# Performance work log

Hardware: AMD Instinct MI355X
Metric: run time of the kernel (lower is better)

Reference implementation:

```python
import jax, jax.numpy as jnp
import numpy as np

B, T, E, H = 4, 2048, 1024, 16
HS = E // H  # 64
EPS = 1e-5


def _layernorm(x, g, b):
    mu = jnp.mean(x, axis=-1, keepdims=True)
    var = jnp.mean(jnp.square(x - mu), axis=-1, keepdims=True)
    return (x - mu) * jax.lax.rsqrt(var + EPS) * g + b


def setup_inputs() -> dict:
    key = jax.random.key(0)
    ks = jax.random.split(key, 12)
    s = 0.02
    return {
        "x": jax.random.normal(ks[0], (B, T, E), dtype=jnp.float32),
        "ln1_g": jnp.ones((E,), jnp.float32),
        "ln1_b": jnp.zeros((E,), jnp.float32),
        "Wq": jax.random.normal(ks[1], (H, E, HS), jnp.float32) * s,
        "Wk": jax.random.normal(ks[2], (H, E, HS), jnp.float32) * s,
        "Wv": jax.random.normal(ks[3], (H, E, HS), jnp.float32) * s,
        "Wo": jax.random.normal(ks[4], (E, E), jnp.float32) * s,
        "bo": jnp.zeros((E,), jnp.float32),
        "ln2_g": jnp.ones((E,), jnp.float32),
        "ln2_b": jnp.zeros((E,), jnp.float32),
        "W1": jax.random.normal(ks[5], (E, 4 * E), jnp.float32) * s,
        "b1": jnp.zeros((4 * E,), jnp.float32),
        "W2": jax.random.normal(ks[6], (4 * E, E), jnp.float32) * s,
        "b2": jnp.zeros((E,), jnp.float32),
    }


def reference(x, ln1_g, ln1_b, Wq, Wk, Wv, Wo, bo, ln2_g, ln2_b, W1, b1, W2, b2):
    # --- self-attention (pre-LN) ---
    h = _layernorm(x, ln1_g, ln1_b)                      # [B,T,E]
    q = jnp.einsum('bte,hed->bhtd', h, Wq)               # [B,H,T,HS]
    k = jnp.einsum('bte,hed->bhtd', h, Wk)
    v = jnp.einsum('bte,hed->bhtd', h, Wv)
    scores = jnp.einsum('bhtd,bhsd->bhts', q, k) * (HS ** -0.5)  # [B,H,T,T]
    att = jax.nn.softmax(scores, axis=-1)
    o = jnp.einsum('bhts,bhsd->bhtd', att, v)            # [B,H,T,HS]
    o = jnp.transpose(o, (0, 2, 1, 3)).reshape(B, T, E)  # concat heads
    x = x + o @ Wo + bo                                  # residual
    # --- feed-forward (pre-LN) ---
    h2 = _layernorm(x, ln2_g, ln2_b)
    x = x + jax.nn.relu(h2 @ W1 + b1) @ W2 + b2
    return x
```

## Files before the change

kernel.cpp:

```cpp
#include <hip/hip_runtime.h>
#include <stdint.h>


typedef __attribute__((ext_vector_type(8))) short s16x8;
typedef __attribute__((ext_vector_type(4))) float f32x4;
typedef unsigned short u16;
typedef __attribute__((ext_vector_type(4))) unsigned short u16x4;

#define XSW(r) ((((r) & 7) ^ (((r) >> 3) & 7)) << 4)

__device__ __forceinline__ u16 f2bf(float f) {
    uint32_t u = __float_as_uint(f);
    u += 0x7fffu + ((u >> 16) & 1u);
    return (u16)(u >> 16);
}
__device__ __forceinline__ float bf2f(u16 u) {
    return __uint_as_float(((uint32_t)u) << 16);
}
__device__ __forceinline__ uint32_t pk2(float a, float b) {
    return (uint32_t)f2bf(a) | ((uint32_t)f2bf(b) << 16);
}
__device__ __forceinline__ float exp2_fast(float x) {
    float r;
    asm("v_exp_f32 %0, %1" : "=v"(r) : "v"(x));
    return r;
}

__device__ __forceinline__ void gld16(const void* g, void* l) {
    __builtin_amdgcn_global_load_lds(
        (const __attribute__((address_space(1))) unsigned int*)g,
        (__attribute__((address_space(3))) unsigned int*)l, 16, 0, 0);
}

__global__ __launch_bounds__(256)
void ln_bf16(const float* __restrict__ x, const float* __restrict__ g,
             const float* __restrict__ bta, u16* __restrict__ y) {
    __shared__ float red[8];
    const int row = blockIdx.x;
    const int t = threadIdx.x;
    const float4 xv = ((const float4*)(x + (size_t)row * 1024))[t];
    float s = xv.x + xv.y + xv.z + xv.w;
    float q = xv.x*xv.x + xv.y*xv.y + xv.z*xv.z + xv.w*xv.w;
#pragma unroll
    for (int off = 32; off; off >>= 1) {
        s += __shfl_down(s, off, 64);
        q += __shfl_down(q, off, 64);
    }
    if ((t & 63) == 0) { red[(t>>6)*2] = s; red[(t>>6)*2+1] = q; }
    __syncthreads();
    const float st = red[0]+red[2]+red[4]+red[6];
    const float qt = red[1]+red[3]+red[5]+red[7];
    const float mu = st * (1.f/1024.f);
    const float rs = rsqrtf(qt*(1.f/1024.f) - mu*mu + 1e-5f);
    const float4 gv = ((const float4*)g)[t];
    const float4 bv = ((const float4*)bta)[t];
    u16x4 o;
    o.x = f2bf((xv.x-mu)*rs*gv.x + bv.x);
    o.y = f2bf((xv.y-mu)*rs*gv.y + bv.y);
    o.z = f2bf((xv.z-mu)*rs*gv.z + bv.z);
    o.w = f2bf((xv.w-mu)*rs*gv.w + bv.w);
    ((u16x4*)(y + (size_t)row*1024))[t] = o;
}

__global__ __launch_bounds__(256)
void transpose_f32_bf16(const float* __restrict__ in, u16* __restrict__ out,
                        int K, int N) {
    __shared__ float tile[64][65];
    const int k0 = blockIdx.x * 64;
    const int n0 = blockIdx.y * 64;
    const int t = threadIdx.x;
    const int r = t >> 2;
    const int c = (t & 3) * 16;
    const float* ip = in + (size_t)(k0 + r) * N + n0 + c;
#pragma unroll
    for (int i = 0; i < 4; ++i) {
        const float4 v = *(const float4*)(ip + i*4);
        tile[r][c+i*4+0]=v.x; tile[r][c+i*4+1]=v.y;
        tile[r][c+i*4+2]=v.z; tile[r][c+i*4+3]=v.w;
    }
    __syncthreads();
    u16 tmp[16] __attribute__((aligned(16)));
#pragma unroll
    for (int i = 0; i < 16; ++i) tmp[i] = f2bf(tile[c+i][r]);
    u16* op = out + (size_t)(n0 + r) * K + k0 + c;
    *(s16x8*)op       = *(const s16x8*)&tmp[0];
    *(s16x8*)(op + 8) = *(const s16x8*)&tmp[8];
}

__global__ __launch_bounds__(256)
void pack_wcat(const float* __restrict__ Wq, const float* __restrict__ Wk,
               const float* __restrict__ Wv, u16* __restrict__ out) {
    __shared__ float tile[64][65];
    const int ph = blockIdx.y;
    const int p = ph >> 4, h = ph & 15;
    const float* W = (p == 0) ? Wq : (p == 1 ? Wk : Wv);
    const float* in = W + (size_t)h * 64 * 1024;
    const int k0 = blockIdx.x * 64;
    const int t = threadIdx.x;
    const int r = t >> 2;
    const int c = (t & 3) * 16;
    const float* ip = in + (size_t)(k0 + r) * 64 + c;
#pragma unroll
    for (int i = 0; i < 4; ++i) {
        const float4 v = *(const float4*)(ip + i*4);
        tile[r][c+i*4+0]=v.x; tile[r][c+i*4+1]=v.y;
        tile[r][c+i*4+2]=v.z; tile[r][c+i*4+3]=v.w;
    }
    __syncthreads();
    u16 tmp[16] __attribute__((aligned(16)));
#pragma unroll
    for (int i = 0; i < 16; ++i) tmp[i] = f2bf(tile[c+i][r]);
    u16* op = out + (size_t)(p*1024 + h*64 + r) * 1024 + k0 + c;
    *(s16x8*)op       = *(const s16x8*)&tmp[0];
    *(s16x8*)(op + 8) = *(const s16x8*)&tmp[8];
}

template<bool RELU, bool HAS_BIAS, bool HAS_RES, bool OUT_BF16, bool SPLIT_V>
__global__ __launch_bounds__(256)
void bgemm(const u16* __restrict__ A, int lda,
           const u16* __restrict__ Bt, int ldb,
           void* Cv, int ldc,
           const float* __restrict__ bias,
           const float* Res, int ldres, int K,
           u16* __restrict__ vT)
{
    __shared__ u16 Als[128*64];
    __shared__ u16 Bls[128*64];
    const int tid = threadIdx.x;
    const int wid = tid >> 6, lane = tid & 63;
    const int bm = blockIdx.y * 128, bn = blockIdx.x * 128;
    const int wr = (wid >> 1) * 64, wc = (wid & 1) * 64;
    const int fr = lane & 15, fq = lane >> 4;
    const int sr8 = lane >> 3, sc8 = (lane & 7) * 8;

    const f32x4 zero = {0.f, 0.f, 0.f, 0.f};
    f32x4 acc[4][4];
#pragma unroll
    for (int m = 0; m < 4; ++m)
#pragma unroll
        for (int n = 0; n < 4; ++n) acc[m][n] = zero;

    const u16* Ap = A  + (size_t)(bm + wid*32 + sr8) * lda + sc8;
    const u16* Bp = Bt + (size_t)(bn + wid*32 + sr8) * ldb + sc8;
    u16* Alp = Als + wid*2048 + lane*8;
    u16* Blp = Bls + wid*2048 + lane*8;

    for (int k0 = 0; k0 < K; k0 += 64) {
#pragma unroll
        for (int c = 0; c < 4; ++c) {
            gld16(Ap + (size_t)(c*8)*lda + k0, Alp + c*512);
            gld16(Bp + (size_t)(c*8)*ldb + k0, Blp + c*512);
        }
        __syncthreads();
#pragma unroll
        for (int kk = 0; kk < 2; ++kk) {
            s16x8 af[4], bf[4];
#pragma unroll
            for (int m = 0; m < 4; ++m)
                af[m] = *(const s16x8*)((const char*)Als + (wr+m*16+fr)*128 + kk*64 + fq*16);
#pragma unroll
            for (int n = 0; n < 4; ++n)
                bf[n] = *(const s16x8*)((const char*)Bls + (wc+n*16+fr)*128 + kk*64 + fq*16);
#pragma unroll
            for (int m = 0; m < 4; ++m)
#pragma unroll
                for (int n = 0; n < 4; ++n)
                    acc[m][n] = __builtin_amdgcn_mfma_f32_16x16x32_bf16(
                        af[m], bf[n], acc[m][n], 0, 0, 0);
        }
        __syncthreads();
    }

    float* Cf = (float*)Cv;
    u16*  Cb = (u16*)Cv;
    if (SPLIT_V && bn >= 2048) {
#pragma unroll
        for (int n = 0; n < 4; ++n) {
            const int local = bn + wc + n*16 + fr - 2048;
            const int hh = local >> 6, dd = local & 63;
#pragma unroll
            for (int m = 0; m < 4; ++m) {
#pragma unroll
                for (int j = 0; j < 4; ++j) {
                    const int row = bm + wr + m*16 + fq*4 + j;
                    const int bb = row >> 11, tt = row & 2047;
                    vT[((size_t)(bb*16 + hh)*64 + dd)*2048 + tt] = f2bf(acc[m][n][j]);
                }
            }
        }
        return;
    }
#pragma unroll
    for (int n = 0; n < 4; ++n) {
        const int col = bn + wc + n*16 + fr;
        const float bval = HAS_BIAS ? bias[col] : 0.f;
#pragma unroll
        for (int m = 0; m < 4; ++m) {
#pragma unroll
            for (int j = 0; j < 4; ++j) {
                const int row = bm + wr + m*16 + fq*4 + j;
                float v = acc[m][n][j] + bval;
                if (HAS_RES) v += Res[(size_t)row * ldres + col];
                if (RELU)    v = fmaxf(v, 0.f);
                if (OUT_BF16) Cb[(size_t)row * ldc + col] = f2bf(v);
                else          Cf[(size_t)row * ldc + col] = v;
            }
        }
    }
}

__global__ __launch_bounds__(256)
void attn_bf16(const u16* __restrict__ qk, const u16* __restrict__ vT,
               u16* __restrict__ out) {
    __shared__ u16 Ks[128*64];
    __shared__ u16 Vt[64*128];
    __shared__ u16 Ps[4][16*128];
    const int b = blockIdx.y >> 4, h = blockIdx.y & 15;
    const int q0 = blockIdx.x << 6;
    const int tid = threadIdx.x;
    const int wid = tid >> 6, lane = tid & 63;
    const int fr = lane & 15, fq = lane >> 4;
    const int srow = tid >> 2;
    const int sce  = (tid & 3) * 16;
    const int vd   = tid >> 4;
    const int vt0  = (tid & 15) * 8;
    const size_t tokbase = (size_t)b * 2048;
    const u16* vbase = vT + (size_t)(b*16 + h) * 64 * 2048;
    const f32x4 zero = {0.f, 0.f, 0.f, 0.f};

    u16* Qst = (u16*)Ps;
    {
        const u16* qp = qk + (tokbase + q0 + srow)*2048 + h*64 + sce;
        const s16x8 v0 = *(const s16x8*)qp;
        const s16x8 v1 = *(const s16x8*)(qp + 8);
        *(s16x8*)((char*)Qst + srow*128 + ((sce*2)      ^ XSW(srow))) = v0;
        *(s16x8*)((char*)Qst + srow*128 + ((sce*2 + 16) ^ XSW(srow))) = v1;
    }
    __syncthreads();
    s16x8 qf[2];
    {
        const int qrow = wid*16 + fr;
        const float qscale = 0.125f * 1.44269504f;
#pragma unroll
        for (int kk = 0; kk < 2; ++kk) {
            const s16x8 raw = *(const s16x8*)((const char*)Qst + qrow*128
                                 + ((kk*64 + fq*16) ^ XSW(qrow)));
#pragma unroll
            for (int i = 0; i < 8; ++i)
                qf[kk][i] = (short)f2bf(bf2f((u16)raw[i]) * qscale);
        }
    }

    float m_run = -1e30f, l_run = 0.f;
    f32x4 oacc[4];
#pragma unroll
    for (int nd = 0; nd < 4; ++nd) oacc[nd] = zero;

    s16x8 kr[4], vr[4];
    {
        const u16* kp0 = qk + (tokbase + srow)*2048 + 1024 + h*64 + sce;
        kr[0] = *(const s16x8*)kp0;
        kr[1] = *(const s16x8*)(kp0 + 8);
        kr[2] = *(const s16x8*)(kp0 + (size_t)64*2048);
        kr[3] = *(const s16x8*)(kp0 + (size_t)64*2048 + 8);
#pragma unroll
        for (int c = 0; c < 4; ++c)
            vr[c] = *(const s16x8*)(vbase + (size_t)(vd + 16*c)*2048 + vt0);
    }

    for (int kt = 0; kt < 2048; kt += 128) {
        __syncthreads();
        {
            const int r0 = srow, r1 = srow + 64;
            *(s16x8*)((char*)Ks + r0*128 + ((sce*2)      ^ XSW(r0))) = kr[0];
            *(s16x8*)((char*)Ks + r0*128 + ((sce*2 + 16) ^ XSW(r0))) = kr[1];
            *(s16x8*)((char*)Ks + r1*128 + ((sce*2)      ^ XSW(r1))) = kr[2];
            *(s16x8*)((char*)Ks + r1*128 + ((sce*2 + 16) ^ XSW(r1))) = kr[3];
        }
#pragma unroll
        for (int c = 0; c < 4; ++c) {
            const int d = vd + 16*c;
            *(s16x8*)((char*)Vt + d*256 + ((vt0*2) ^ XSW(d))) = vr[c];
        }
        __syncthreads();

        if (kt + 128 < 2048) {
            const u16* kp0 = qk + (tokbase + kt + 128 + srow)*2048 + 1024 + h*64 + sce;
            kr[0] = *(const s16x8*)kp0;
            kr[1] = *(const s16x8*)(kp0 + 8);
            kr[2] = *(const s16x8*)(kp0 + (size_t)64*2048);
            kr[3] = *(const s16x8*)(kp0 + (size_t)64*2048 + 8);
#pragma unroll
            for (int c = 0; c < 4; ++c)
                vr[c] = *(const s16x8*)(vbase + (size_t)(vd + 16*c)*2048
                                        + kt + 128 + vt0);
        }

        f32x4 sv[8];
        __builtin_amdgcn_s_setprio(1);
#pragma unroll
        for (int n = 0; n < 8; ++n) {
            sv[n] = zero;
            const int r = n*16 + fr;
#pragma unroll
            for (int kk = 0; kk < 2; ++kk) {
                const s16x8 kf = *(const s16x8*)((const char*)Ks + r*128
                                     + ((kk*64 + fq*16) ^ XSW(r)));
                sv[n] = __builtin_amdgcn_mfma_f32_16x16x32_bf16(kf, qf[kk], sv[n], 0,0,0);
            }
        }
        __builtin_amdgcn_s_setprio(0);

        float pv[32];
        float mx = -1e30f;
#pragma unroll
        for (int n = 0; n < 8; ++n)
#pragma unroll
            for (int j = 0; j < 4; ++j) {
                const float s = sv[n][j];
                pv[n*4 + j] = s;
                mx = fmaxf(mx, s);
            }
        mx = fmaxf(mx, __shfl_xor(mx, 16, 64));
        mx = fmaxf(mx, __shfl_xor(mx, 32, 64));
        const float mn = fmaxf(m_run, mx);
        const float al = exp2_fast(m_run - mn);
        m_run = mn;
        float rs = 0.f;
#pragma unroll
        for (int t = 0; t < 32; ++t) { pv[t] = exp2_fast(pv[t] - mn); rs += pv[t]; }
        rs += __shfl_xor(rs, 16, 64);
        rs += __shfl_xor(rs, 32, 64);
        l_run = l_run * al + rs;
#pragma unroll
        for (int nd = 0; nd < 4; ++nd)
#pragma unroll
            for (int j = 0; j < 4; ++j) oacc[nd][j] *= al;

        u16* Pw = (u16*)Ps + wid*2048;
#pragma unroll
        for (int n = 0; n < 8; ++n) {
            const uint64_t w = (uint64_t)pk2(pv[n*4+0], pv[n*4+1])
                             | ((uint64_t)pk2(pv[n*4+2], pv[n*4+3]) << 32);
            *(uint64_t*)((char*)Pw + fr*256 + ((n*32 + fq*8) ^ XSW(fr))) = w;
        }
        asm volatile("s_waitcnt lgkmcnt(0)" ::: "memory");
        __builtin_amdgcn_sched_barrier(0);

        s16x8 pf[4];
#pragma unroll
        for (int k2 = 0; k2 < 4; ++k2)
            pf[k2] = *(const s16x8*)((const char*)Pw + fr*256
                         + ((k2*64 + fq*16) ^ XSW(fr)));
        __builtin_amdgcn_s_setprio(1);
#pragma unroll
        for (int nd = 0; nd < 4; ++nd) {
            const int d = nd*16 + fr;
#pragma unroll
            for (int k2 = 0; k2 < 4; ++k2) {
                const s16x8 vf = *(const s16x8*)((const char*)Vt + d*256
                                     + ((k2*64 + fq*16) ^ XSW(d)));
                oacc[nd] = __builtin_amdgcn_mfma_f32_16x16x32_bf16(vf, pf[k2], oacc[nd], 0,0,0);
            }
        }
        __builtin_amdgcn_s_setprio(0);
    }

    const float inv = 1.0f / l_run;
    const size_t row = tokbase + q0 + wid*16 + fr;
#pragma unroll
    for (int nd = 0; nd < 4; ++nd) {
        u16x4 o;
#pragma unroll
        for (int j = 0; j < 4; ++j) o[j] = f2bf(oacc[nd][j] * inv);
        *(u16x4*)(out + row*1024 + h*64 + nd*16 + fq*4) = o;
    }
}

extern "C" void kernel_launch(void* const* d_in, const int* in_sizes, int n_in,
                              void* d_out, int out_size, void* d_ws, size_t ws_size,
                              hipStream_t stream) {
    (void)in_sizes; (void)n_in; (void)out_size; (void)ws_size;
    const float* x     = (const float*)d_in[0];
    const float* ln1_g = (const float*)d_in[1];
    const float* ln1_b = (const float*)d_in[2];
    const float* Wq    = (const float*)d_in[3];
    const float* Wk    = (const float*)d_in[4];
    const float* Wv    = (const float*)d_in[5];
    const float* Wo    = (const float*)d_in[6];
    const float* bo    = (const float*)d_in[7];
    const float* ln2_g = (const float*)d_in[8];
    const float* ln2_b = (const float*)d_in[9];
    const float* W1    = (const float*)d_in[10];
    const float* b1    = (const float*)d_in[11];
    const float* W2    = (const float*)d_in[12];
    const float* b2    = (const float*)d_in[13];
    float* out = (float*)d_out;

    char* w = (char*)d_ws;
    u16* WcatT = (u16*)w;  w += (size_t)3072*1024*2;
    u16* WoT   = (u16*)w;  w += (size_t)1024*1024*2;
    u16* W1T   = (u16*)w;  w += (size_t)4096*1024*2;
    u16* W2T   = (u16*)w;  w += (size_t)1024*4096*2;
    u16* hb    = (u16*)w;  w += (size_t)8192*1024*2;
    u16* qkb   = (u16*)w;  w += (size_t)8192*2048*2;
    u16* vTb   = (u16*)w;  w += (size_t)64*64*2048*2;
    u16* attno = (u16*)w;  w += (size_t)8192*1024*2;
    u16* a1    = (u16*)w;  w += (size_t)8192*4096*2;

    pack_wcat<<<dim3(16, 48), 256, 0, stream>>>(Wq, Wk, Wv, WcatT);
    transpose_f32_bf16<<<dim3(16, 16), 256, 0, stream>>>(Wo, WoT, 1024, 1024);
    transpose_f32_bf16<<<dim3(16, 64), 256, 0, stream>>>(W1, W1T, 1024, 4096);
    transpose_f32_bf16<<<dim3(64, 16), 256, 0, stream>>>(W2, W2T, 4096, 1024);

    ln_bf16<<<dim3(8192), 256, 0, stream>>>(x, ln1_g, ln1_b, hb);
    bgemm<false,false,false,true,true><<<dim3(24, 64), 256, 0, stream>>>(
        hb, 1024, WcatT, 1024, qkb, 2048, nullptr, nullptr, 0, 1024, vTb);
    attn_bf16<<<dim3(32, 64), 256, 0, stream>>>(qkb, vTb, attno);
    bgemm<false,true,true,false,false><<<dim3(8, 64), 256, 0, stream>>>(
        attno, 1024, WoT, 1024, out, 1024, bo, x, 1024, 1024, nullptr);
    ln_bf16<<<dim3(8192), 256, 0, stream>>>(out, ln2_g, ln2_b, hb);
    bgemm<true,true,false,true,false><<<dim3(32, 64), 256, 0, stream>>>(
        hb, 1024, W1T, 1024, a1, 4096, b1, nullptr, 0, 1024, nullptr);
    bgemm<false,true,true,false,false><<<dim3(8, 64), 256, 0, stream>>>(
        a1, 4096, W2T, 4096, out, 1024, b2, out, 1024, 4096, nullptr);
}
```

Measured before the change: 640.5 us.

## Load attention K/V directly from global, remap blocks for L2 locality, use hw bf16 pack

The attention kernel no longer stages K and V tiles through LDS with barriers. Each wave reads its MFMA fragments straight from global memory and relies on L2 reuse, with blocks of the same head remapped so they run close together in time. The GEMM block index is also remapped for L2 locality. Online softmax now rescales only when the running max grows by more than a threshold, and bf16 packing uses the hardware cvt_pk instruction. The risks are uncoalesced global fragment loads in place of LDS reads, and possible L2 or XCD locality effects from the remapping.

```diff
diff --git a/kernel.cpp b/kernel.cpp
--- a/kernel.cpp
+++ b/kernel.cpp
@@ -17,8 +17,10 @@
 __device__ __forceinline__ float bf2f(u16 u) {
     return __uint_as_float(((uint32_t)u) << 16);
 }
-__device__ __forceinline__ uint32_t pk2(float a, float b) {
-    return (uint32_t)f2bf(a) | ((uint32_t)f2bf(b) << 16);
+__device__ __forceinline__ uint32_t cvtpk(float a, float b) {
+    uint32_t r;
+    asm("v_cvt_pk_bf16_f32 %0, %1, %2" : "=v"(r) : "v"(a), "v"(b));
+    return r;
 }
 __device__ __forceinline__ float exp2_fast(float x) {
     float r;
@@ -54,12 +56,10 @@
     const float rs = rsqrtf(qt*(1.f/1024.f) - mu*mu + 1e-5f);
     const float4 gv = ((const float4*)g)[t];
     const float4 bv = ((const float4*)bta)[t];
-    u16x4 o;
-    o.x = f2bf((xv.x-mu)*rs*gv.x + bv.x);
-    o.y = f2bf((xv.y-mu)*rs*gv.y + bv.y);
-    o.z = f2bf((xv.z-mu)*rs*gv.z + bv.z);
-    o.w = f2bf((xv.w-mu)*rs*gv.w + bv.w);
-    ((u16x4*)(y + (size_t)row*1024))[t] = o;
+    uint32_t w0 = cvtpk((xv.x-mu)*rs*gv.x + bv.x, (xv.y-mu)*rs*gv.y + bv.y);
+    uint32_t w1 = cvtpk((xv.z-mu)*rs*gv.z + bv.z, (xv.w-mu)*rs*gv.w + bv.w);
+    uint2 o; o.x = w0; o.y = w1;
+    ((uint2*)(y + (size_t)row*1024))[t] = o;
 }
 
 __global__ __launch_bounds__(256)
@@ -128,7 +128,10 @@
     __shared__ u16 Bls[128*64];
     const int tid = threadIdx.x;
     const int wid = tid >> 6, lane = tid & 63;
-    const int bm = blockIdx.y * 128, bn = blockIdx.x * 128;
+    const int lin = blockIdx.y * gridDim.x + blockIdx.x;
+    const int qx = gridDim.x >> 3;
+    const int bn = ((lin & 7)*qx + ((lin >> 3) % qx)) * 128;
+    const int bm = ((lin >> 3) / qx) * 128;
     const int wr = (wid >> 1) * 64, wc = (wid & 1) * 64;
     const int fr = lane & 15, fq = lane >> 4;
     const int sr8 = lane >> 3, sc8 = (lane & 7) * 8;
@@ -212,42 +215,32 @@
 __global__ __launch_bounds__(256)
 void attn_bf16(const u16* __restrict__ qk, const u16* __restrict__ vT,
                u16* __restrict__ out) {
-    __shared__ u16 Ks[128*64];
-    __shared__ u16 Vt[64*128];
     __shared__ u16 Ps[4][16*128];
-    const int b = blockIdx.y >> 4, h = blockIdx.y & 15;
-    const int q0 = blockIdx.x << 6;
+    const int lin = blockIdx.x;
+    const int bh = (lin & 7)*8 + ((lin >> 3) & 7);
+    const int qb = lin >> 6;
+    const int b = bh >> 4, h = bh & 15;
+    const int q0 = qb << 6;
     const int tid = threadIdx.x;
     const int wid = tid >> 6, lane = tid & 63;
     const int fr = lane & 15, fq = lane >> 4;
-    const int srow = tid >> 2;
-    const int sce  = (tid & 3) * 16;
-    const int vd   = tid >> 4;
-    const int vt0  = (tid & 15) * 8;
     const size_t tokbase = (size_t)b * 2048;
     const u16* vbase = vT + (size_t)(b*16 + h) * 64 * 2048;
     const f32x4 zero = {0.f, 0.f, 0.f, 0.f};
-
-    u16* Qst = (u16*)Ps;
-    {
-        const u16* qp = qk + (tokbase + q0 + srow)*2048 + h*64 + sce;
-        const s16x8 v0 = *(const s16x8*)qp;
-        const s16x8 v1 = *(const s16x8*)(qp + 8);
-        *(s16x8*)((char*)Qst + srow*128 + ((sce*2)      ^ XSW(srow))) = v0;
-        *(s16x8*)((char*)Qst + srow*128 + ((sce*2 + 16) ^ XSW(srow))) = v1;
-    }
-    __syncthreads();
+    const float THR = 10.0f;
+
     s16x8 qf[2];
     {
-        const int qrow = wid*16 + fr;
-        const float qscale = 0.125f * 1.44269504f;
+        const u16* qp = qk + (tokbase + q0 + wid*16 + fr)*2048 + h*64;
+        const float qs = 0.125f * 1.44269504f;
 #pragma unroll
         for (int kk = 0; kk < 2; ++kk) {
-            const s16x8 raw = *(const s16x8*)((const char*)Qst + qrow*128
-                                 + ((kk*64 + fq*16) ^ XSW(qrow)));
-#pragma unroll
-            for (int i = 0; i < 8; ++i)
-                qf[kk][i] = (short)f2bf(bf2f((u16)raw[i]) * qscale);
+            const s16x8 raw = *(const s16x8*)(qp + kk*32 + fq*8);
+            union { s16x8 v; uint32_t w[4]; } u;
+#pragma unroll
+            for (int i = 0; i < 4; ++i)
+                u.w[i] = cvtpk(bf2f((u16)raw[2*i])*qs, bf2f((u16)raw[2*i+1])*qs);
+            qf[kk] = u.v;
         }
     }
 
@@ -256,56 +249,17 @@
 #pragma unroll
     for (int nd = 0; nd < 4; ++nd) oacc[nd] = zero;
 
-    s16x8 kr[4], vr[4];
-    {
-        const u16* kp0 = qk + (tokbase + srow)*2048 + 1024 + h*64 + sce;
-        kr[0] = *(const s16x8*)kp0;
-        kr[1] = *(const s16x8*)(kp0 + 8);
-        kr[2] = *(const s16x8*)(kp0 + (size_t)64*2048);
-        kr[3] = *(const s16x8*)(kp0 + (size_t)64*2048 + 8);
-#pragma unroll
-        for (int c = 0; c < 4; ++c)
-            vr[c] = *(const s16x8*)(vbase + (size_t)(vd + 16*c)*2048 + vt0);
-    }
-
     for (int kt = 0; kt < 2048; kt += 128) {
-        __syncthreads();
-        {
-            const int r0 = srow, r1 = srow + 64;
-            *(s16x8*)((char*)Ks + r0*128 + ((sce*2)      ^ XSW(r0))) = kr[0];
-            *(s16x8*)((char*)Ks + r0*128 + ((sce*2 + 16) ^ XSW(r0))) = kr[1];
-            *(s16x8*)((char*)Ks + r1*128 + ((sce*2)      ^ XSW(r1))) = kr[2];
-            *(s16x8*)((char*)Ks + r1*128 + ((sce*2 + 16) ^ XSW(r1))) = kr[3];
-        }
-#pragma unroll
-        for (int c = 0; c < 4; ++c) {
-            const int d = vd + 16*c;
-            *(s16x8*)((char*)Vt + d*256 + ((vt0*2) ^ XSW(d))) = vr[c];
-        }
-        __syncthreads();
-
-        if (kt + 128 < 2048) {
-            const u16* kp0 = qk + (tokbase + kt + 128 + srow)*2048 + 1024 + h*64 + sce;
-            kr[0] = *(const s16x8*)kp0;
-            kr[1] = *(const s16x8*)(kp0 + 8);
-            kr[2] = *(const s16x8*)(kp0 + (size_t)64*2048);
-            kr[3] = *(const s16x8*)(kp0 + (size_t)64*2048 + 8);
-#pragma unroll
-            for (int c = 0; c < 4; ++c)
-                vr[c] = *(const s16x8*)(vbase + (size_t)(vd + 16*c)*2048
-                                        + kt + 128 + vt0);
-        }
-
+        const u16* kp = qk + (tokbase + kt + fr)*2048 + 1024 + h*64 + fq*8;
         f32x4 sv[8];
         __builtin_amdgcn_s_setprio(1);
 #pragma unroll
         for (int n = 0; n < 8; ++n) {
             sv[n] = zero;
-            const int r = n*16 + fr;
+            const u16* kr = kp + (size_t)(n*16)*2048;
 #pragma unroll
             for (int kk = 0; kk < 2; ++kk) {
-                const s16x8 kf = *(const s16x8*)((const char*)Ks + r*128
-                                     + ((kk*64 + fq*16) ^ XSW(r)));
+                const s16x8 kf = *(const s16x8*)(kr + kk*32);
                 sv[n] = __builtin_amdgcn_mfma_f32_16x16x32_bf16(kf, qf[kk], sv[n], 0,0,0);
             }
         }
@@ -323,25 +277,27 @@
             }
         mx = fmaxf(mx, __shfl_xor(mx, 16, 64));
         mx = fmaxf(mx, __shfl_xor(mx, 32, 64));
-        const float mn = fmaxf(m_run, mx);
-        const float al = exp2_fast(m_run - mn);
-        m_run = mn;
+        if (mx > m_run + THR) {
+            const float al = exp2_fast(m_run - mx);
+            m_run = mx;
+            l_run *= al;
+#pragma unroll
+            for (int nd = 0; nd < 4; ++nd)
+#pragma unroll
+                for (int j = 0; j < 4; ++j) oacc[nd][j] *= al;
+        }
         float rs = 0.f;
 #pragma unroll
-        for (int t = 0; t < 32; ++t) { pv[t] = exp2_fast(pv[t] - mn); rs += pv[t]; }
+        for (int t = 0; t < 32; ++t) { pv[t] = exp2_fast(pv[t] - m_run); rs += pv[t]; }
         rs += __shfl_xor(rs, 16, 64);
         rs += __shfl_xor(rs, 32, 64);
-        l_run = l_run * al + rs;
-#pragma unroll
-        for (int nd = 0; nd < 4; ++nd)
-#pragma unroll
-            for (int j = 0; j < 4; ++j) oacc[nd][j] *= al;
+        l_run += rs;
 
         u16* Pw = (u16*)Ps + wid*2048;
 #pragma unroll
         for (int n = 0; n < 8; ++n) {
-            const uint64_t w = (uint64_t)pk2(pv[n*4+0], pv[n*4+1])
-                             | ((uint64_t)pk2(pv[n*4+2], pv[n*4+3]) << 32);
+            const uint64_t w = (uint64_t)cvtpk(pv[n*4+0], pv[n*4+1])
+                             | ((uint64_t)cvtpk(pv[n*4+2], pv[n*4+3]) << 32);
             *(uint64_t*)((char*)Pw + fr*256 + ((n*32 + fq*8) ^ XSW(fr))) = w;
         }
         asm volatile("s_waitcnt lgkmcnt(0)" ::: "memory");
@@ -352,14 +308,14 @@
         for (int k2 = 0; k2 < 4; ++k2)
             pf[k2] = *(const s16x8*)((const char*)Pw + fr*256
                          + ((k2*64 + fq*16) ^ XSW(fr)));
+        const u16* vp = vbase + (size_t)fr*2048 + kt + fq*8;
         __builtin_amdgcn_s_setprio(1);
 #pragma unroll
         for (int nd = 0; nd < 4; ++nd) {
-            const int d = nd*16 + fr;
+            const u16* vr = vp + (size_t)(nd*16)*2048;
 #pragma unroll
             for (int k2 = 0; k2 < 4; ++k2) {
-                const s16x8 vf = *(const s16x8*)((const char*)Vt + d*256
-                                     + ((k2*64 + fq*16) ^ XSW(d)));
+                const s16x8 vf = *(const s16x8*)(vr + k2*32);
                 oacc[nd] = __builtin_amdgcn_mfma_f32_16x16x32_bf16(vf, pf[k2], oacc[nd], 0,0,0);
             }
         }
@@ -370,10 +326,10 @@
     const size_t row = tokbase + q0 + wid*16 + fr;
 #pragma unroll
     for (int nd = 0; nd < 4; ++nd) {
-        u16x4 o;
-#pragma unroll
-        for (int j = 0; j < 4; ++j) o[j] = f2bf(oacc[nd][j] * inv);
-        *(u16x4*)(out + row*1024 + h*64 + nd*16 + fq*4) = o;
+        uint2 o;
+        o.x = cvtpk(oacc[nd][0]*inv, oacc[nd][1]*inv);
+        o.y = cvtpk(oacc[nd][2]*inv, oacc[nd][3]*inv);
+        *(uint2*)(out + row*1024 + h*64 + nd*16 + fq*4) = o;
     }
 }
 
@@ -416,7 +372,7 @@
     ln_bf16<<<dim3(8192), 256, 0, stream>>>(x, ln1_g, ln1_b, hb);
     bgemm<false,false,false,true,true><<<dim3(24, 64), 256, 0, stream>>>(
         hb, 1024, WcatT, 1024, qkb, 2048, nullptr, nullptr, 0, 1024, vTb);
-    attn_bf16<<<dim3(32, 64), 256, 0, stream>>>(qkb, vTb, attno);
+    attn_bf16<<<dim3(2048), 256, 0, stream>>>(qkb, vTb, attno);
     bgemm<false,true,true,false,false><<<dim3(8, 64), 256, 0, stream>>>(
         attno, 1024, WoT, 1024, out, 1024, bo, x, 1024, 1024, nullptr);
     ln_bf16<<<dim3(8192), 256, 0, stream>>>(out, ln2_g, ln2_b, hb);
```

New measurement: 939.5 us. 46.7% more time.
